# Kernel optimization log

Hardware: AMD Instinct MI355X
Metric: run time of the kernel (lower is better)

## Reference

```python
import jax, jax.numpy as jnp
import numpy as np
from jax import lax

H = 32  # hidden size


def _lstm_layer(x, Wih, Whh, bih, bhh):
    """x: [B, T, D_in]; returns [B, T, H]. PyTorch gate order i,f,g,o."""
    B = x.shape[0]
    b = bih + bhh  # [4H]
    # precompute input projections for all timesteps: [T, B, 4H]
    xp = jnp.einsum('btd,gd->tbg', x, Wih) + b

    def step(carry, xt):
        h, c = carry
        gates = xt + h @ Whh.T  # [B, 4H]
        i, f, g, o = jnp.split(gates, 4, axis=-1)
        i = jax.nn.sigmoid(i)
        f = jax.nn.sigmoid(f)
        g = jnp.tanh(g)
        o = jax.nn.sigmoid(o)
        c = f * c + i * g
        h = o * jnp.tanh(c)
        return (h, c), h

    init = (jnp.zeros((B, H), x.dtype), jnp.zeros((B, H), x.dtype))
    _, ys = lax.scan(step, init, xp)  # ys: [T, B, H]
    return jnp.swapaxes(ys, 0, 1)


def _lstm5(x, Wih0, Wih_rest, Whh, bih, bhh):
    h = _lstm_layer(x, Wih0, Whh[0], bih[0], bhh[0])
    for l in range(4):  # fixed small layer count
        h = _lstm_layer(h, Wih_rest[l], Whh[l + 1], bih[l + 1], bhh[l + 1])
    return h


def setup_inputs() -> dict:
    key = jax.random.key(0)
    ks = jax.random.split(key, 18)
    s = 1.0 / np.sqrt(H)
    B, T = 16384, 20
    u = lambda k, shp: jax.random.uniform(k, shp, jnp.float32, -s, s)
    return {
        'accel': jax.random.normal(ks[0], (B, T, 3), jnp.float32),
        'gyro': jax.random.normal(ks[1], (B, T, 3), jnp.float32),
        'accel_Wih0': u(ks[2], (4 * H, 3)),
        'accel_Wih_rest': u(ks[3], (4, 4 * H, H)),
        'accel_Whh': u(ks[4], (5, 4 * H, H)),
        'accel_bih': u(ks[5], (5, 4 * H)),
        'accel_bhh': u(ks[6], (5, 4 * H)),
        'gyro_Wih0': u(ks[7], (4 * H, 3)),
        'gyro_Wih_rest': u(ks[8], (4, 4 * H, H)),
        'gyro_Whh': u(ks[9], (5, 4 * H, H)),
        'gyro_bih': u(ks[10], (5, 4 * H)),
        'gyro_bhh': u(ks[11], (5, 4 * H)),
        'fc1_w': u(ks[12], (128, T * H * 2)),
        'fc1_b': u(ks[13], (128,)),
        'fc2_w': u(ks[14], (5, 128)),
        'fc2_b': u(ks[15], (5,)),
    }


def reference(accel, gyro, accel_Wih0, accel_Wih_rest, accel_Whh, accel_bih,
              accel_bhh, gyro_Wih0, gyro_Wih_rest, gyro_Whh, gyro_bih,
              gyro_bhh, fc1_w, fc1_b, fc2_w, fc2_b):
    a = _lstm5(accel, accel_Wih0, accel_Wih_rest, accel_Whh, accel_bih, accel_bhh)
    g = _lstm5(gyro, gyro_Wih0, gyro_Wih_rest, gyro_Whh, gyro_bih, gyro_bhh)
    x = jnp.concatenate([a, g], axis=1)          # [B, 2T, H]
    x = x.reshape(x.shape[0], -1)                # [B, 2*T*H]
    x = jax.nn.relu(x @ fc1_w.T + fc1_b)         # [B, 128]
    return x @ fc2_w.T + fc2_b                   # [B, 5]
```

## Files before the change

kernel.cpp:

```cpp
#include <hip/hip_runtime.h>
#include <math.h>

#define B_TOTAL 16384
#define T_STEPS 20
#define NGRP    1024

typedef __attribute__((ext_vector_type(8))) __bf16 bf16x8;
typedef __attribute__((ext_vector_type(4))) float f32x4;

__device__ __forceinline__ __bf16 bf16_bits(unsigned short s) {
    __bf16 r; __builtin_memcpy(&r, &s, 2); return r;
}
__device__ __forceinline__ void split_trunc(float x, __bf16& hi, __bf16& lo) {
    unsigned u = __float_as_uint(x);
    hi = bf16_bits((unsigned short)(u >> 16));
    float l = x - __uint_as_float(u & 0xFFFF0000u);
    lo = bf16_bits((unsigned short)(__float_as_uint(l) >> 16));
}

__global__ __launch_bounds__(256, 4)
void lstm5_mfma(const float* __restrict__ accel, const float* __restrict__ gyro,
                const float* __restrict__ aWih0, const float* __restrict__ aWihR,
                const float* __restrict__ aWhh,  const float* __restrict__ aBih,
                const float* __restrict__ aBhh,
                const float* __restrict__ gWih0, const float* __restrict__ gWihR,
                const float* __restrict__ gWhh,  const float* __restrict__ gBih,
                const float* __restrict__ gBhh,
                const float* __restrict__ fc1_w,
                __bf16* __restrict__ w1ah, __bf16* __restrict__ w1al,
                __bf16* __restrict__ Xhi, __bf16* __restrict__ Xlo) {
    const int tid  = threadIdx.x;
    const int w    = tid >> 6;
    const int lane = tid & 63;
    const int e    = lane & 15;
    const int quad = lane >> 4;
    const int sensor = blockIdx.y;
    const int bbase  = blockIdx.x * 16;

    if (sensor == 0 && blockIdx.x < 80) {
        int idx = blockIdx.x * 256 + tid;
        int plane = idx & 63;
        int ks    = (idx >> 6) % 40;
        int mt    = idx / (64 * 40);
        int row   = mt * 16 + (plane & 15);
        int col0  = ks * 32 + (plane >> 4) * 8;
        const float* src = fc1_w + row * 1280 + col0;
#pragma unroll
        for (int j = 0; j < 8; ++j) {
            __bf16 h_, l_;
            split_trunc(src[j], h_, l_);
            w1ah[(size_t)idx * 8 + j] = h_;
            w1al[(size_t)idx * 8 + j] = l_;
        }
    }

    const float* xin  = sensor ? gyro  : accel;
    const float* Wih0 = sensor ? gWih0 : aWih0;
    const float* WihR = sensor ? gWihR : aWihR;
    const float* Whh  = sensor ? gWhh  : aWhh;
    const float* Bih  = sensor ? gBih  : aBih;
    const float* Bhh  = sensor ? gBhh  : aBhh;

    __shared__ __align__(16) __bf16 shi[20 * 512];
    __shared__ __align__(16) __bf16 slo[20 * 512];

    const int ug0 = w * 8 + quad;
    const int ug1 = w * 8 + 4 + quad;

    const int m_row   = lane & 15;
    const int orow_t0 = (m_row & 3) * 32 + (w * 8 + (m_row >> 2));
    const int orow_t1 = (m_row & 3) * 32 + (w * 8 + 4 + (m_row >> 2));

    bf16x8 wih_h0, wih_l0, wih_h1, wih_l1;
    bf16x8 whh_h0, whh_l0, whh_h1, whh_l1;
    f32x4  bias0v, bias1v;
    float  c0 = 0.f, c1 = 0.f;

#define LOAD_FRAG(Wsrc, orow, fh, fl)                         \
    {                                                         \
        const float* p_ = (Wsrc) + (orow) * 32 + quad * 8;    \
        _Pragma("unroll")                                     \
        for (int jj = 0; jj < 8; ++jj) {                      \
            __bf16 h_, l_;                                    \
            split_trunc(p_[jj], h_, l_);                      \
            (fh)[jj] = h_;  (fl)[jj] = l_;                    \
        }                                                     \
    }

#define LOAD_BIAS(l)                                                        \
    {                                                                       \
        _Pragma("unroll")                                                   \
        for (int r = 0; r < 4; ++r) {                                       \
            bias0v[r] = Bih[(l) * 128 + r * 32 + ug0] + Bhh[(l) * 128 + r * 32 + ug0]; \
            bias1v[r] = Bih[(l) * 128 + r * 32 + ug1] + Bhh[(l) * 128 + r * 32 + ug1]; \
        }                                                                   \
    }

#define ACT_STORE(t)                                                        \
    {                                                                       \
        float d1 = 1.f + __expf(fminf(-acc0[0], 17.f));                     \
        float d2 = 1.f + __expf(fminf(-acc0[1], 17.f));                     \
        float d3 = 1.f + __expf(fminf(2.f * acc0[2], 17.f));                \
        float d4 = 1.f + __expf(fminf(-acc0[3], 17.f));                     \
        float p2 = d1 * d2, p3 = p2 * d3, P = p3 * d4;                      \
        float s3 = d3 * d4, s2 = d2 * s3;                                   \
        float R  = __builtin_amdgcn_rcpf(P);                                \
        float i0 = R * s2;                                                  \
        float f0 = R * d1 * s3;                                             \
        float g0 = fmaf(-2.f, R * p2 * d4, 1.f);                            \
        float o0 = R * p3;                                                  \
        c0 = fmaf(f0, c0, i0 * g0);                                         \
        float e1 = 1.f + __expf(fminf(-acc1[0], 17.f));                     \
        float e2 = 1.f + __expf(fminf(-acc1[1], 17.f));                     \
        float e3 = 1.f + __expf(fminf(2.f * acc1[2], 17.f));                \
        float e4 = 1.f + __expf(fminf(-acc1[3], 17.f));                     \
        float q2 = e1 * e2, q3 = q2 * e3, Q = q3 * e4;                      \
        float u3 = e3 * e4, u2 = e2 * u3;                                   \
        float S  = __builtin_amdgcn_rcpf(Q);                                \
        float i1 = S * u2;                                                  \
        float f1 = S * e1 * u3;                                             \
        float g1 = fmaf(-2.f, S * q2 * e4, 1.f);                            \
        float o1 = S * q3;                                                  \
        c1 = fmaf(f1, c1, i1 * g1);                                         \
        float d9 = 1.f + __expf(fminf(2.f * c0, 30.f));                     \
        float da = 1.f + __expf(fminf(2.f * c1, 30.f));                     \
        float R2 = __builtin_amdgcn_rcpf(d9 * da);                          \
        float h0 = fmaf(-2.f, o0 * (R2 * da), o0);                          \
        float h1 = fmaf(-2.f, o1 * (R2 * d9), o1);                          \
        __syncthreads();             \
        int i0x = (t) * 512 + w * 128 + e * 8 + quad;                       \
        int i1x = i0x + 4;                                                  \
        __bf16 hh_, ll_;                                                    \
        split_trunc(h0, hh_, ll_);  shi[i0x] = hh_;  slo[i0x] = ll_;        \
        split_trunc(h1, hh_, ll_);  shi[i1x] = hh_;  slo[i1x] = ll_;        \
        __syncthreads();       \
    }

    {
        LOAD_FRAG(Whh, orow_t0, whh_h0, whh_l0);
        LOAD_FRAG(Whh, orow_t1, whh_h1, whh_l1);
        LOAD_BIAS(0);
        float w0reg[2][4][3];
#pragma unroll
        for (int r = 0; r < 4; ++r)
#pragma unroll
            for (int k = 0; k < 3; ++k) {
                w0reg[0][r][k] = Wih0[(r * 32 + ug0) * 3 + k];
                w0reg[1][r][k] = Wih0[(r * 32 + ug1) * 3 + k];
            }
        const float* xrow = xin + (size_t)(bbase + e) * (T_STEPS * 3);

        for (int t = 0; t < T_STEPS; ++t) {
            float x0 = xrow[t * 3 + 0];
            float x1 = xrow[t * 3 + 1];
            float x2 = xrow[t * 3 + 2];
            f32x4 acc0 = bias0v;
            f32x4 acc1 = bias1v;
#pragma unroll
            for (int r = 0; r < 4; ++r) {
                acc0[r] = fmaf(w0reg[0][r][0], x0,
                          fmaf(w0reg[0][r][1], x1,
                          fmaf(w0reg[0][r][2], x2, acc0[r])));
                acc1[r] = fmaf(w0reg[1][r][0], x0,
                          fmaf(w0reg[1][r][1], x1,
                          fmaf(w0reg[1][r][2], x2, acc1[r])));
            }
            if (t > 0) {
                int rb = (t - 1) * 512 + quad * 128 + e * 8;
                bf16x8 bh = *(const bf16x8*)&shi[rb];
                bf16x8 bl = *(const bf16x8*)&slo[rb];
                acc0 = __builtin_amdgcn_mfma_f32_16x16x32_bf16(whh_h0, bh, acc0, 0, 0, 0);
                acc0 = __builtin_amdgcn_mfma_f32_16x16x32_bf16(whh_h0, bl, acc0, 0, 0, 0);
                acc0 = __builtin_amdgcn_mfma_f32_16x16x32_bf16(whh_l0, bh, acc0, 0, 0, 0);
                acc1 = __builtin_amdgcn_mfma_f32_16x16x32_bf16(whh_h1, bh, acc1, 0, 0, 0);
                acc1 = __builtin_amdgcn_mfma_f32_16x16x32_bf16(whh_h1, bl, acc1, 0, 0, 0);
                acc1 = __builtin_amdgcn_mfma_f32_16x16x32_bf16(whh_l1, bh, acc1, 0, 0, 0);
            }
            ACT_STORE(t);
        }
    }

    for (int l = 1; l < 5; ++l) {
        const float* Wi = WihR + (l - 1) * 4096;
        const float* Wh = Whh + l * 4096;
        LOAD_FRAG(Wi, orow_t0, wih_h0, wih_l0);
        LOAD_FRAG(Wi, orow_t1, wih_h1, wih_l1);
        LOAD_FRAG(Wh, orow_t0, whh_h0, whh_l0);
        LOAD_FRAG(Wh, orow_t1, whh_h1, whh_l1);
        LOAD_BIAS(l);
        c0 = 0.f; c1 = 0.f;

        for (int t = 0; t < T_STEPS; ++t) {
            f32x4 acc0, acc1;
            {
                int rb = t * 512 + quad * 128 + e * 8;
                bf16x8 bh = *(const bf16x8*)&shi[rb];
                bf16x8 bl = *(const bf16x8*)&slo[rb];
                acc0 = __builtin_amdgcn_mfma_f32_16x16x32_bf16(wih_h0, bh, bias0v, 0, 0, 0);
                acc0 = __builtin_amdgcn_mfma_f32_16x16x32_bf16(wih_h0, bl, acc0, 0, 0, 0);
                acc0 = __builtin_amdgcn_mfma_f32_16x16x32_bf16(wih_l0, bh, acc0, 0, 0, 0);
                acc1 = __builtin_amdgcn_mfma_f32_16x16x32_bf16(wih_h1, bh, bias1v, 0, 0, 0);
                acc1 = __builtin_amdgcn_mfma_f32_16x16x32_bf16(wih_h1, bl, acc1, 0, 0, 0);
                acc1 = __builtin_amdgcn_mfma_f32_16x16x32_bf16(wih_l1, bh, acc1, 0, 0, 0);
            }
            if (t > 0) {
                int rb = (t - 1) * 512 + quad * 128 + e * 8;
                bf16x8 bh = *(const bf16x8*)&shi[rb];
                bf16x8 bl = *(const bf16x8*)&slo[rb];
                acc0 = __builtin_amdgcn_mfma_f32_16x16x32_bf16(whh_h0, bh, acc0, 0, 0, 0);
                acc0 = __builtin_amdgcn_mfma_f32_16x16x32_bf16(whh_h0, bl, acc0, 0, 0, 0);
                acc0 = __builtin_amdgcn_mfma_f32_16x16x32_bf16(whh_l0, bh, acc0, 0, 0, 0);
                acc1 = __builtin_amdgcn_mfma_f32_16x16x32_bf16(whh_h1, bh, acc1, 0, 0, 0);
                acc1 = __builtin_amdgcn_mfma_f32_16x16x32_bf16(whh_h1, bl, acc1, 0, 0, 0);
                acc1 = __builtin_amdgcn_mfma_f32_16x16x32_bf16(whh_l1, bh, acc1, 0, 0, 0);
            }
            ACT_STORE(t);
        }
    }
    __syncthreads();

    {
        size_t base = ((size_t)(sensor * NGRP + blockIdx.x)) * (20 * 512);
        float4* dh = (float4*)(Xhi + base);
        float4* dl = (float4*)(Xlo + base);
        const float4* sh = (const float4*)shi;
        const float4* sl = (const float4*)slo;
        for (int i = tid; i < 20 * 512 / 8; i += 256) { dh[i] = sh[i]; dl[i] = sl[i]; }
    }
#undef LOAD_FRAG
#undef LOAD_BIAS
#undef ACT_STORE
}

__global__ __launch_bounds__(256, 2)
void fc_mfma(const __bf16* __restrict__ Xhi, const __bf16* __restrict__ Xlo,
             const __bf16* __restrict__ w1ah, const __bf16* __restrict__ w1al,
             const float* __restrict__ fc1_b, const float* __restrict__ fc2_w,
             const float* __restrict__ fc2_b, float* __restrict__ out) {
    const int tid  = threadIdx.x;
    const int wv   = tid >> 6;
    const int lane = tid & 63;
    const int e    = lane & 15;
    const int quad = lane >> 4;
    const int kv   = wv & 1;
    const int mv   = wv >> 1;
    const int g0   = blockIdx.x * 2;

    __shared__ __align__(16) f32x4 sacc[2][4][2][64];
    __shared__ float sred[2][2][16][5];

    f32x4 acc[4][2];
#pragma unroll
    for (int m = 0; m < 4; ++m)
#pragma unroll
        for (int cg = 0; cg < 2; ++cg) acc[m][cg] = (f32x4){0.f, 0.f, 0.f, 0.f};

    for (int kk = 0; kk < 20; ++kk) {
        int ks = kv * 20 + kk;
        bf16x8 bh[2], bl[2];
#pragma unroll
        for (int cg = 0; cg < 2; ++cg) {
            size_t bb = ((size_t)(kv * NGRP + g0 + cg)) * (20 * 512) + kk * 512 + lane * 8;
            bh[cg] = *(const bf16x8*)(Xhi + bb);
            bl[cg] = *(const bf16x8*)(Xlo + bb);
        }
#pragma unroll
        for (int m = 0; m < 4; ++m) {
            int mt = mv * 4 + m;
            size_t ab = ((size_t)((mt * 40 + ks) * 64 + lane)) * 8;
            bf16x8 ah = *(const bf16x8*)(w1ah + ab);
            bf16x8 al = *(const bf16x8*)(w1al + ab);
#pragma unroll
            for (int cg = 0; cg < 2; ++cg) {
                acc[m][cg] = __builtin_amdgcn_mfma_f32_16x16x32_bf16(ah, bh[cg], acc[m][cg], 0, 0, 0);
                acc[m][cg] = __builtin_amdgcn_mfma_f32_16x16x32_bf16(ah, bl[cg], acc[m][cg], 0, 0, 0);
                acc[m][cg] = __builtin_amdgcn_mfma_f32_16x16x32_bf16(al, bh[cg], acc[m][cg], 0, 0, 0);
            }
        }
    }

    if (kv == 1) {
#pragma unroll
        for (int m = 0; m < 4; ++m)
#pragma unroll
            for (int cg = 0; cg < 2; ++cg) sacc[mv][m][cg][lane] = acc[m][cg];
    }
    __syncthreads();

    if (kv == 0) {
        float p[2][5];
#pragma unroll
        for (int cg = 0; cg < 2; ++cg)
#pragma unroll
            for (int n = 0; n < 5; ++n) p[cg][n] = 0.f;
#pragma unroll
        for (int m = 0; m < 4; ++m) {
            int mt = mv * 4 + m;
#pragma unroll
            for (int cg = 0; cg < 2; ++cg) {
                f32x4 z  = acc[m][cg];
                f32x4 zz = sacc[mv][m][cg][lane];
#pragma unroll
                for (int r = 0; r < 4; ++r) {
                    int row = mt * 16 + quad * 4 + r;
                    float v = fmaxf(z[r] + zz[r] + fc1_b[row], 0.f);
#pragma unroll
                    for (int n = 0; n < 5; ++n)
                        p[cg][n] = fmaf(v, fc2_w[n * 128 + row], p[cg][n]);
                }
            }
        }
#pragma unroll
        for (int cg = 0; cg < 2; ++cg)
#pragma unroll
            for (int n = 0; n < 5; ++n) {
                p[cg][n] += __shfl_xor(p[cg][n], 16, 64);
                p[cg][n] += __shfl_xor(p[cg][n], 32, 64);
            }
        if (quad == 0) {
#pragma unroll
            for (int cg = 0; cg < 2; ++cg)
#pragma unroll
                for (int n = 0; n < 5; ++n) sred[mv][cg][e][n] = p[cg][n];
        }
    }
    __syncthreads();
    if (tid < 160) {
        int col = tid / 5, n = tid - col * 5;
        out[((size_t)(blockIdx.x * 32 + col)) * 5 + n] =
            sred[0][col >> 4][col & 15][n] + sred[1][col >> 4][col & 15][n] + fc2_b[n];
    }
}

extern "C" void kernel_launch(void* const* d_in, const int* in_sizes, int n_in,
                              void* d_out, int out_size, void* d_ws, size_t ws_size,
                              hipStream_t stream) {
    const float* accel  = (const float*)d_in[0];
    const float* gyro   = (const float*)d_in[1];
    const float* aWih0  = (const float*)d_in[2];
    const float* aWihR  = (const float*)d_in[3];
    const float* aWhh   = (const float*)d_in[4];
    const float* aBih   = (const float*)d_in[5];
    const float* aBhh   = (const float*)d_in[6];
    const float* gWih0  = (const float*)d_in[7];
    const float* gWihR  = (const float*)d_in[8];
    const float* gWhh   = (const float*)d_in[9];
    const float* gBih   = (const float*)d_in[10];
    const float* gBhh   = (const float*)d_in[11];
    const float* fc1_w  = (const float*)d_in[12];
    const float* fc1_b  = (const float*)d_in[13];
    const float* fc2_w  = (const float*)d_in[14];
    const float* fc2_b  = (const float*)d_in[15];
    float* out = (float*)d_out;

    const size_t XN = (size_t)2 * NGRP * 20 * 512;
    __bf16* Xhi  = (__bf16*)d_ws;
    __bf16* Xlo  = Xhi + XN;
    __bf16* W1ah = Xlo + XN;
    __bf16* W1al = W1ah + 163840;

    hipLaunchKernelGGL(lstm5_mfma, dim3(NGRP, 2), dim3(256), 0, stream,
                       accel, gyro, aWih0, aWihR, aWhh, aBih, aBhh,
                       gWih0, gWihR, gWhh, gBih, gBhh,
                       fc1_w, W1ah, W1al, Xhi, Xlo);

    hipLaunchKernelGGL(fc_mfma, dim3(B_TOTAL / 32), dim3(256), 0, stream,
                       Xhi, Xlo, W1ah, W1al, fc1_b, fc2_w, fc2_b, out);
}
```

Measured before the change: 321.6 us.

## Use sliding LDS window to drop a barrier per step and fold log2e into weights

The shared-memory h buffer grows to 24 slots, and each layer writes its outputs one slot below where it reads. This lets a single __syncthreads per timestep replace the earlier pair of barriers around the store. Gate weights and biases are pre-scaled by log2e (2*log2e for the g gate) so the activations can call exp2 directly without clamps. The sigmoid/tanh algebra now uses two reciprocals per unit instead of one combined product, and adjacent hidden units are packed into 32-bit LDS stores. Occupancy hint drops from 4 to 3 blocks per CU because of the larger LDS footprint, and removing the clamps risks overflow to inf on extreme inputs.

```diff
diff --git a/kernel.cpp b/kernel.cpp
--- a/kernel.cpp
+++ b/kernel.cpp
@@ -4,6 +4,9 @@
 #define B_TOTAL 16384
 #define T_STEPS 20
 #define NGRP    1024
+
+#define LOG2E    1.44269504088896f
+#define TWOLOG2E 2.88539008177793f
 
 typedef __attribute__((ext_vector_type(8))) __bf16 bf16x8;
 typedef __attribute__((ext_vector_type(4))) float f32x4;
@@ -18,7 +21,7 @@
     lo = bf16_bits((unsigned short)(__float_as_uint(l) >> 16));
 }
 
-__global__ __launch_bounds__(256, 4)
+__global__ __launch_bounds__(256, 3)
 void lstm5_mfma(const float* __restrict__ accel, const float* __restrict__ gyro,
                 const float* __restrict__ aWih0, const float* __restrict__ aWihR,
                 const float* __restrict__ aWhh,  const float* __restrict__ aBih,
@@ -61,15 +64,16 @@
     const float* Bih  = sensor ? gBih  : aBih;
     const float* Bhh  = sensor ? gBhh  : aBhh;
 
-    __shared__ __align__(16) __bf16 shi[20 * 512];
-    __shared__ __align__(16) __bf16 slo[20 * 512];
-
-    const int ug0 = w * 8 + quad;
-    const int ug1 = w * 8 + 4 + quad;
+    __shared__ __align__(16) __bf16 shi[24 * 512];
+    __shared__ __align__(16) __bf16 slo[24 * 512];
+
+    const int ug0 = w * 8 + 2 * quad;
+    const int ug1 = w * 8 + 2 * quad + 1;
 
     const int m_row   = lane & 15;
-    const int orow_t0 = (m_row & 3) * 32 + (w * 8 + (m_row >> 2));
-    const int orow_t1 = (m_row & 3) * 32 + (w * 8 + 4 + (m_row >> 2));
+    const int orow_t0 = (m_row & 3) * 32 + (w * 8 + 2 * (m_row >> 2));
+    const int orow_t1 = orow_t0 + 1;
+    const float sA = ((m_row & 3) == 2) ? TWOLOG2E : LOG2E;
 
     bf16x8 wih_h0, wih_l0, wih_h1, wih_l1;
     bf16x8 whh_h0, whh_l0, whh_h1, whh_l1;
@@ -82,7 +86,7 @@
         _Pragma("unroll")                                     \
         for (int jj = 0; jj < 8; ++jj) {                      \
             __bf16 h_, l_;                                    \
-            split_trunc(p_[jj], h_, l_);                      \
+            split_trunc(p_[jj] * sA, h_, l_);                 \
             (fh)[jj] = h_;  (fl)[jj] = l_;                    \
         }                                                     \
     }
@@ -91,49 +95,47 @@
     {                                                                       \
         _Pragma("unroll")                                                   \
         for (int r = 0; r < 4; ++r) {                                       \
-            bias0v[r] = Bih[(l) * 128 + r * 32 + ug0] + Bhh[(l) * 128 + r * 32 + ug0]; \
-            bias1v[r] = Bih[(l) * 128 + r * 32 + ug1] + Bhh[(l) * 128 + r * 32 + ug1]; \
+            float sc = (r == 2) ? TWOLOG2E : LOG2E;                         \
+            bias0v[r] = (Bih[(l) * 128 + r * 32 + ug0] + Bhh[(l) * 128 + r * 32 + ug0]) * sc; \
+            bias1v[r] = (Bih[(l) * 128 + r * 32 + ug1] + Bhh[(l) * 128 + r * 32 + ug1]) * sc; \
         }                                                                   \
     }
 
-#define ACT_STORE(t)                                                        \
+#define ACT_STORE(wslot)                                                    \
     {                                                                       \
-        float d1 = 1.f + __expf(fminf(-acc0[0], 17.f));                     \
-        float d2 = 1.f + __expf(fminf(-acc0[1], 17.f));                     \
-        float d3 = 1.f + __expf(fminf(2.f * acc0[2], 17.f));                \
-        float d4 = 1.f + __expf(fminf(-acc0[3], 17.f));                     \
-        float p2 = d1 * d2, p3 = p2 * d3, P = p3 * d4;                      \
-        float s3 = d3 * d4, s2 = d2 * s3;                                   \
-        float R  = __builtin_amdgcn_rcpf(P);                                \
-        float i0 = R * s2;                                                  \
-        float f0 = R * d1 * s3;                                             \
-        float g0 = fmaf(-2.f, R * p2 * d4, 1.f);                            \
-        float o0 = R * p3;                                                  \
+        float d1 = 1.f + __builtin_exp2f(-acc0[0]);                         \
+        float d2 = 1.f + __builtin_exp2f(-acc0[1]);                         \
+        float d3 = 1.f + __builtin_exp2f( acc0[2]);                         \
+        float d4 = 1.f + __builtin_exp2f(-acc0[3]);                         \
+        float R12 = __builtin_amdgcn_rcpf(d1 * d2);                         \
+        float R34 = __builtin_amdgcn_rcpf(d3 * d4);                         \
+        float i0 = R12 * d2, f0 = R12 * d1;                                 \
+        float g0 = fmaf(-2.f, R34 * d4, 1.f);                               \
+        float o0 = R34 * d3;                                                \
         c0 = fmaf(f0, c0, i0 * g0);                                         \
-        float e1 = 1.f + __expf(fminf(-acc1[0], 17.f));                     \
-        float e2 = 1.f + __expf(fminf(-acc1[1], 17.f));                     \
-        float e3 = 1.f + __expf(fminf(2.f * acc1[2], 17.f));                \
-        float e4 = 1.f + __expf(fminf(-acc1[3], 17.f));                     \
-        float q2 = e1 * e2, q3 = q2 * e3, Q = q3 * e4;                      \
-        float u3 = e3 * e4, u2 = e2 * u3;                                   \
-        float S  = __builtin_amdgcn_rcpf(Q);                                \
-        float i1 = S * u2;                                                  \
-        float f1 = S * e1 * u3;                                             \
-        float g1 = fmaf(-2.f, S * q2 * e4, 1.f);                            \
-        float o1 = S * q3;                                                  \
+        float e1 = 1.f + __builtin_exp2f(-acc1[0]);                         \
+        float e2 = 1.f + __builtin_exp2f(-acc1[1]);                         \
+        float e3 = 1.f + __builtin_exp2f( acc1[2]);                         \
+        float e4 = 1.f + __builtin_exp2f(-acc1[3]);                         \
+        float S12 = __builtin_amdgcn_rcpf(e1 * e2);                         \
+        float S34 = __builtin_amdgcn_rcpf(e3 * e4);                         \
+        float i1 = S12 * e2, f1 = S12 * e1;                                 \
+        float g1 = fmaf(-2.f, S34 * e4, 1.f);                               \
+        float o1 = S34 * e3;                                                \
         c1 = fmaf(f1, c1, i1 * g1);                                         \
-        float d9 = 1.f + __expf(fminf(2.f * c0, 30.f));                     \
-        float da = 1.f + __expf(fminf(2.f * c1, 30.f));                     \
-        float R2 = __builtin_amdgcn_rcpf(d9 * da);                          \
-        float h0 = fmaf(-2.f, o0 * (R2 * da), o0);                          \
-        float h1 = fmaf(-2.f, o1 * (R2 * d9), o1);                          \
-        __syncthreads();             \
-        int i0x = (t) * 512 + w * 128 + e * 8 + quad;                       \
-        int i1x = i0x + 4;                                                  \
-        __bf16 hh_, ll_;                                                    \
-        split_trunc(h0, hh_, ll_);  shi[i0x] = hh_;  slo[i0x] = ll_;        \
-        split_trunc(h1, hh_, ll_);  shi[i1x] = hh_;  slo[i1x] = ll_;        \
-        __syncthreads();       \
+        float d9 = 1.f + __builtin_exp2f(c0 * TWOLOG2E);                    \
+        float da = 1.f + __builtin_exp2f(c1 * TWOLOG2E);                    \
+        float Rc = __builtin_amdgcn_rcpf(d9 * da);                          \
+        float h0 = fmaf(-2.f * o0, Rc * da, o0);                            \
+        float h1 = fmaf(-2.f * o1, Rc * d9, o1);                            \
+        unsigned u0 = __float_as_uint(h0), u1 = __float_as_uint(h1);        \
+        float l0 = h0 - __uint_as_float(u0 & 0xFFFF0000u);                  \
+        float l1 = h1 - __uint_as_float(u1 & 0xFFFF0000u);                  \
+        int ix = (wslot) * 512 + w * 128 + e * 8 + 2 * quad;                \
+        *(unsigned*)(shi + ix) = (u0 >> 16) | (u1 & 0xFFFF0000u);           \
+        *(unsigned*)(slo + ix) = (__float_as_uint(l0) >> 16) |              \
+                                 (__float_as_uint(l1) & 0xFFFF0000u);       \
+        __syncthreads();    \
     }
 
     {
@@ -142,12 +144,14 @@
         LOAD_BIAS(0);
         float w0reg[2][4][3];
 #pragma unroll
-        for (int r = 0; r < 4; ++r)
+        for (int r = 0; r < 4; ++r) {
+            float sc = (r == 2) ? TWOLOG2E : LOG2E;
 #pragma unroll
             for (int k = 0; k < 3; ++k) {
-                w0reg[0][r][k] = Wih0[(r * 32 + ug0) * 3 + k];
-                w0reg[1][r][k] = Wih0[(r * 32 + ug1) * 3 + k];
-            }
+                w0reg[0][r][k] = Wih0[(r * 32 + ug0) * 3 + k] * sc;
+                w0reg[1][r][k] = Wih0[(r * 32 + ug1) * 3 + k] * sc;
+            }
+        }
         const float* xrow = xin + (size_t)(bbase + e) * (T_STEPS * 3);
 
         for (int t = 0; t < T_STEPS; ++t) {
@@ -166,7 +170,7 @@
                           fmaf(w0reg[1][r][2], x2, acc1[r])));
             }
             if (t > 0) {
-                int rb = (t - 1) * 512 + quad * 128 + e * 8;
+                int rb = (4 + t - 1) * 512 + quad * 128 + e * 8;
                 bf16x8 bh = *(const bf16x8*)&shi[rb];
                 bf16x8 bl = *(const bf16x8*)&slo[rb];
                 acc0 = __builtin_amdgcn_mfma_f32_16x16x32_bf16(whh_h0, bh, acc0, 0, 0, 0);
@@ -176,11 +180,12 @@
                 acc1 = __builtin_amdgcn_mfma_f32_16x16x32_bf16(whh_h1, bl, acc1, 0, 0, 0);
                 acc1 = __builtin_amdgcn_mfma_f32_16x16x32_bf16(whh_l1, bh, acc1, 0, 0, 0);
             }
-            ACT_STORE(t);
+            ACT_STORE(4 + t);
         }
     }
 
     for (int l = 1; l < 5; ++l) {
+        const int o = 4 - l;
         const float* Wi = WihR + (l - 1) * 4096;
         const float* Wh = Whh + l * 4096;
         LOAD_FRAG(Wi, orow_t0, wih_h0, wih_l0);
@@ -193,7 +198,7 @@
         for (int t = 0; t < T_STEPS; ++t) {
             f32x4 acc0, acc1;
             {
-                int rb = t * 512 + quad * 128 + e * 8;
+                int rb = (o + 1 + t) * 512 + quad * 128 + e * 8;
                 bf16x8 bh = *(const bf16x8*)&shi[rb];
                 bf16x8 bl = *(const bf16x8*)&slo[rb];
                 acc0 = __builtin_amdgcn_mfma_f32_16x16x32_bf16(wih_h0, bh, bias0v, 0, 0, 0);
@@ -204,7 +209,7 @@
                 acc1 = __builtin_amdgcn_mfma_f32_16x16x32_bf16(wih_l1, bh, acc1, 0, 0, 0);
             }
             if (t > 0) {
-                int rb = (t - 1) * 512 + quad * 128 + e * 8;
+                int rb = (o + t - 1) * 512 + quad * 128 + e * 8;
                 bf16x8 bh = *(const bf16x8*)&shi[rb];
                 bf16x8 bl = *(const bf16x8*)&slo[rb];
                 acc0 = __builtin_amdgcn_mfma_f32_16x16x32_bf16(whh_h0, bh, acc0, 0, 0, 0);
@@ -214,10 +219,9 @@
                 acc1 = __builtin_amdgcn_mfma_f32_16x16x32_bf16(whh_h1, bl, acc1, 0, 0, 0);
                 acc1 = __builtin_amdgcn_mfma_f32_16x16x32_bf16(whh_l1, bh, acc1, 0, 0, 0);
             }
-            ACT_STORE(t);
-        }
-    }
-    __syncthreads();
+            ACT_STORE(o + t);
+        }
+    }
 
     {
         size_t base = ((size_t)(sensor * NGRP + blockIdx.x)) * (20 * 512);
```

After: 347.7 us. 1.08x slower.
